# Performance work log

Measured on AMD Instinct MI355X. Metric: run time of the kernel, lower is better.

Reference implementation:

```python
import jax, jax.numpy as jnp
import numpy as np

N_HEAD = 12

def setup_inputs() -> dict:
    key = jax.random.key(0)
    k1, k2, k3 = jax.random.split(key, 3)
    B, T, C = 8, 1024, 768
    x = jax.random.normal(k1, (B, T, C), dtype=jnp.float32)
    # torch nn.Linear weight layout: [out_features, in_features]
    W_attn = jax.random.normal(k2, (3 * C, C), dtype=jnp.float32) * 0.02
    b_attn = jax.random.normal(k3, (3 * C,), dtype=jnp.float32) * 0.02
    return {"x": x, "W_attn": W_attn, "b_attn": b_attn}

def reference(x, W_attn, b_attn):
    B, T, C = x.shape
    H = N_HEAD
    hs = C // H
    scale = 1.0 / jnp.sqrt(jnp.asarray(hs, x.dtype))
    # fused qkv projection: x @ W^T + b  -> [B, T, 3C]
    qkv = jnp.einsum('btc,oc->bto', x, W_attn) + b_attn
    qkv = qkv.reshape(B, T, 3, H, hs).transpose(2, 0, 3, 1, 4)  # [3, B, H, T, hs]
    q, k, v = qkv[0], qkv[1], qkv[2]
    scores = jnp.einsum('bhqd,bhkd->bhqk', q, k) * scale  # [B, H, T, T]
    causal = jnp.tril(jnp.ones((T, T), dtype=bool))
    # masked_fill(-inf) followed by ReLU == zero out masked positions after ReLU
    att = jnp.where(causal, jax.nn.relu(scores), jnp.zeros((), scores.dtype))
    y = jnp.einsum('bhqk,bhkd->bhqd', att, v)  # [B, H, T, hs]
    return y.transpose(0, 2, 1, 3).reshape(B, T, C)
```

## Files before the change

kernel.cpp:

```cpp
#include <hip/hip_runtime.h>
#include <hip/hip_bf16.h>
#include <stdint.h>

#define T_ 1024
#define C_ 768
#define H_ 12
#define HS 64

typedef __attribute__((ext_vector_type(8))) short bf16x8;
typedef __attribute__((ext_vector_type(4))) float f32x4;
typedef __attribute__((ext_vector_type(16))) float f32x16;

#define GLOAD16(g, l) __builtin_amdgcn_global_load_lds( \
    (const __attribute__((address_space(1))) uint32_t*)(g), \
    (__attribute__((address_space(3))) uint32_t*)(l), 16, 0, 0)

#define WAITCNT_VM(n) asm volatile("s_waitcnt vmcnt(" #n ")" ::: "memory")

__device__ __forceinline__ ushort f2b(float f) {
  uint32_t u = __builtin_bit_cast(uint32_t, f);
  u = (u + 0x7fffu + ((u >> 16) & 1u)) >> 16;
  return (ushort)u;
}

__device__ __forceinline__ uint cvtpk(float a, float b) {
  uint r;
  asm("v_cvt_pk_bf16_f32 %0, %1, %2" : "=v"(r) : "v"(a), "v"(b));
  return r;
}

__global__ __launch_bounds__(256) void cvt_bf16(
    const float* __restrict__ x, const float* __restrict__ wt,
    ushort* __restrict__ xb, ushort* __restrict__ wb) {
  const int NX4 = 8192 * 768 / 4;
  const int NW4 = 2304 * 768 / 4;
  int i = blockIdx.x * 256 + threadIdx.x;
  int stride = gridDim.x * 256;
  for (int idx = i; idx < NX4; idx += stride) {
    float4 f = ((const float4*)x)[idx];
    ushort4 o;
    o.x = f2b(f.x); o.y = f2b(f.y); o.z = f2b(f.z); o.w = f2b(f.w);
    ((ushort4*)xb)[idx] = o;
  }
  for (int idx = i; idx < NW4; idx += stride) {
    float4 f = ((const float4*)wt)[idx];
    ushort4 o;
    o.x = f2b(f.x); o.y = f2b(f.y); o.z = f2b(f.z); o.w = f2b(f.w);
    ((ushort4*)wb)[idx] = o;
  }
}

__global__ __launch_bounds__(256) void qkv_gemm(
    const ushort* __restrict__ xb, const ushort* __restrict__ wb,
    const float* __restrict__ bias,
    ushort* __restrict__ qo, ushort* __restrict__ ko, ushort* __restrict__ vT) {
  __shared__ __align__(16) char smem[81920];
  const int tid = threadIdx.x, lane = tid & 63, w = tid >> 6;
  const int g = lane >> 4, l15 = lane & 15;
  const int id = blockIdx.x;
  const int wg = (id & 7) * 144 + (id >> 3);
  const int m0 = (wg / 18) * 128, n0 = (wg % 18) * 128;
  const int wr = w >> 1, wc = w & 1;
  f32x4 acc[4][4] = {};

  const ushort* srcA[2];
  const ushort* srcB[2];
  int dstoff[2];
  #pragma unroll
  for (int c = 0; c < 2; ++c) {
    int p = (c * 4 + w) * 64 + lane;
    int row = p >> 2, s = p & 3;
    int sc = (s ^ ((row >> 1) & 3)) * 8;
    srcA[c] = xb + (size_t)(m0 + row) * 768 + sc;
    srcB[c] = wb + (size_t)(n0 + row) * 768 + sc;
    dstoff[c] = (c * 4 + w) * 1024;
  }

#define STAGE_G(bb_, k0) do { \
    _Pragma("unroll") \
    for (int c_ = 0; c_ < 2; ++c_) { \
      GLOAD16(srcA[c_] + (k0), (bb_) + dstoff[c_]); \
      GLOAD16(srcB[c_] + (k0), (bb_) + 8192 + dstoff[c_]); \
    } \
  } while (0)

#define GEMM_COMPUTE(cb_) do { \
    bf16x8 af[4], bfr[4]; \
    _Pragma("unroll") \
    for (int mi = 0; mi < 4; ++mi) { \
      int r_ = wr * 64 + mi * 16 + l15; \
      af[mi] = *(const bf16x8*)((cb_) + r_ * 64 + ((g ^ ((r_ >> 1) & 3)) << 4)); \
    } \
    _Pragma("unroll") \
    for (int ni = 0; ni < 4; ++ni) { \
      int r_ = wc * 64 + ni * 16 + l15; \
      bfr[ni] = *(const bf16x8*)((cb_) + 8192 + r_ * 64 + ((g ^ ((r_ >> 1) & 3)) << 4)); \
    } \
    __builtin_amdgcn_s_setprio(1); \
    _Pragma("unroll") \
    for (int mi = 0; mi < 4; ++mi) \
      _Pragma("unroll") \
      for (int ni = 0; ni < 4; ++ni) \
        acc[mi][ni] = __builtin_amdgcn_mfma_f32_16x16x32_bf16(af[mi], bfr[ni], acc[mi][ni], 0, 0, 0); \
    __builtin_amdgcn_s_setprio(0); \
  } while (0)

  STAGE_G(smem, 0);
  STAGE_G(smem + 16384, 32);
  STAGE_G(smem + 32768, 64);
  STAGE_G(smem + 49152, 96);
  char* cptr = smem;
  char* sptr = smem + 65536;
  for (int kk = 0; kk < 23; ++kk) {
    if (kk <= 20)      WAITCNT_VM(12);
    else if (kk == 21) WAITCNT_VM(8);
    else               WAITCNT_VM(4);
    __builtin_amdgcn_s_barrier();
    if (kk < 20) STAGE_G(sptr, (kk + 4) * 32);
    GEMM_COMPUTE(cptr);
    cptr += 16384; if (cptr == smem + 81920) cptr = smem;
    sptr += 16384; if (sptr == smem + 81920) sptr = smem;
  }
  WAITCNT_VM(0);
  __builtin_amdgcn_s_barrier();
  GEMM_COMPUTE(cptr);
  __syncthreads();

  const int which = n0 / 768;
  if (which < 2) {
    ushort* outp = (which == 0) ? qo : ko;
    #pragma unroll
    for (int ni = 0; ni < 4; ++ni) {
      float bn = bias[n0 + wc * 64 + ni * 16 + l15];
      int nl = wc * 64 + ni * 16 + l15;
      #pragma unroll
      for (int mi = 0; mi < 4; ++mi) {
        #pragma unroll
        for (int r = 0; r < 4; ++r) {
          int ml = wr * 64 + mi * 16 + g * 4 + r;
          *(ushort*)(smem + ml * 256 + ((nl * 2) ^ ((ml & 7) << 4))) =
              f2b(acc[mi][ni][r] + bn);
        }
      }
    }
    __syncthreads();
    #pragma unroll
    for (int c = 0; c < 8; ++c) {
      int p = c * 256 + tid;
      int ml = p >> 4, nch = p & 15;
      uint4 val = *(const uint4*)(smem + ml * 256 + ((nch * 16) ^ ((ml & 7) << 4)));
      int m = m0 + ml;
      int nin = n0 + nch * 8 - which * 768;
      int h = nin >> 6, d = nin & 63;
      *(uint4*)(outp + ((size_t)((m >> 10) * H_ + h) * T_ + (m & (T_ - 1))) * HS + d) = val;
    }
  } else {
    #pragma unroll
    for (int ni = 0; ni < 4; ++ni) {
      float bn = bias[n0 + wc * 64 + ni * 16 + l15];
      int dl = wc * 64 + ni * 16 + l15;
      #pragma unroll
      for (int mi = 0; mi < 4; ++mi) {
        #pragma unroll
        for (int r = 0; r < 4; ++r) {
          int tl = wr * 64 + mi * 16 + g * 4 + r;
          *(ushort*)(smem + dl * 256 + ((tl * 2) ^ ((dl & 7) << 4))) =
              f2b(acc[mi][ni][r] + bn);
        }
      }
    }
    __syncthreads();
    const int b = m0 >> 10, t0base = m0 & 1023;
    #pragma unroll
    for (int c = 0; c < 8; ++c) {
      int p = c * 256 + tid;
      int dl = p >> 4, tch = p & 15;
      uint4 val = *(const uint4*)(smem + dl * 256 + ((tch * 16) ^ ((dl & 7) << 4)));
      int nin = n0 + dl - 1536;
      int h = nin >> 6, dd = nin & 63;
      *(uint4*)(vT + (((size_t)(b * H_ + h) * HS + dd) << 10) + t0base + tch * 8) = val;
    }
  }
}

__global__ __launch_bounds__(512, 4) void attn_relu(
    const ushort* __restrict__ q, const ushort* __restrict__ k,
    const ushort* __restrict__ vT, float* __restrict__ out) {
  __shared__ __align__(16) char smem[49152];
  const int tid = threadIdx.x, lane = tid & 63, w = tid >> 6;
  const int l31 = lane & 31, h = lane >> 5;
  const int raw = blockIdx.x;
  const int chunk = 3 - (raw / 96);
  const int bh = raw % 96;
  const size_t base = (size_t)bh * (T_ * HS);
  const int q0w = chunk * 256 + w * 32;
  const int nkt = chunk * 4 + 4;

  bf16x8 qf[4];
  #pragma unroll
  for (int s = 0; s < 4; ++s)
    qf[s] = *(const bf16x8*)(q + base + (size_t)(q0w + l31) * HS + s * 16 + h * 8);

  const int rowS = tid >> 3;
  const int colS = ((tid & 7) ^ (rowS & 7)) * 8;
  const int dstS = tid * 16;

#define STAGE_KV(bb_, kt) do { \
    GLOAD16(k  + base + (size_t)((kt) * 64 + rowS) * HS + colS, (bb_) + dstS); \
    GLOAD16(vT + base + (size_t)rowS * T_ + (kt) * 64 + colS, (bb_) + 8192 + dstS); \
  } while (0)

  f32x16 yacc0 = {}, yacc1 = {};

#define ATTN_TILE(cb_, kt) do { \
    const char* Kb = (cb_); \
    const char* Vb = (cb_) + 8192; \
    _Pragma("unroll") \
    for (int kr = 0; kr < 2; ++kr) { \
      int kbase = (kt) * 64 + kr * 32; \
      if (kbase <= q0w + 31) { \
        f32x16 sacc = {}; \
        int arow = kr * 32 + l31; \
        __builtin_amdgcn_s_setprio(1); \
        _Pragma("unroll") \
        for (int s = 0; s < 4; ++s) { \
          bf16x8 kf = *(const bf16x8*)(Kb + arow * 128 + (((2 * s + h) ^ (arow & 7)) << 4)); \
          sacc = __builtin_amdgcn_mfma_f32_32x32x16_bf16(kf, qf[s], sacc, 0, 0, 0); \
        } \
        __builtin_amdgcn_s_setprio(0); \
        const bool fullk = (kbase + 31 <= q0w); \
        uint wds[8]; \
        _Pragma("unroll") \
        for (int i = 0; i < 8; ++i) { \
          float a = fmaxf(sacc[2 * i] * 0.125f, 0.0f); \
          float b = fmaxf(sacc[2 * i + 1] * 0.125f, 0.0f); \
          if (!fullk) { \
            int r0 = 2 * i, r1 = 2 * i + 1; \
            if (kbase + (r0 & 3) + 8 * (r0 >> 2) + 4 * h > q0w + l31) a = 0.0f; \
            if (kbase + (r1 & 3) + 8 * (r1 >> 2) + 4 * h > q0w + l31) b = 0.0f; \
          } \
          wds[i] = cvtpk(a, b); \
        } \
        __builtin_amdgcn_s_setprio(1); \
        _Pragma("unroll") \
        for (int t = 0; t < 2; ++t) { \
          int4 pw = { (int)wds[4 * t], (int)wds[4 * t + 1], \
                      (int)wds[4 * t + 2], (int)wds[4 * t + 3] }; \
          bf16x8 pa = __builtin_bit_cast(bf16x8, pw); \
          _Pragma("unroll") \
          for (int dt = 0; dt < 2; ++dt) { \
            int d = dt * 32 + l31; \
            uint2 lo = *(const uint2*)(Vb + d * 128 + (((4 * kr + 2 * t) ^ (d & 7)) << 4) + 8 * h); \
            uint2 hi = *(const uint2*)(Vb + d * 128 + (((4 * kr + 2 * t + 1) ^ (d & 7)) << 4) + 8 * h); \
            int4 vv = { (int)lo.x, (int)lo.y, (int)hi.x, (int)hi.y }; \
            bf16x8 vf = __builtin_bit_cast(bf16x8, vv); \
            if (dt == 0) yacc0 = __builtin_amdgcn_mfma_f32_32x32x16_bf16(pa, vf, yacc0, 0, 0, 0); \
            else         yacc1 = __builtin_amdgcn_mfma_f32_32x32x16_bf16(pa, vf, yacc1, 0, 0, 0); \
          } \
        } \
        __builtin_amdgcn_s_setprio(0); \
      } \
    } \
  } while (0)

  STAGE_KV(smem, 0);
  if (nkt > 1) STAGE_KV(smem + 16384, 1);
  char* cptr = smem;
  char* sptr = smem + 32768;
  for (int kt = 0; kt < nkt - 1; ++kt) {
    WAITCNT_VM(2);
    __builtin_amdgcn_s_barrier();
    if (kt + 2 < nkt) STAGE_KV(sptr, kt + 2);
    ATTN_TILE(cptr, kt);
    cptr += 16384; if (cptr == smem + 49152) cptr = smem;
    sptr += 16384; if (sptr == smem + 49152) sptr = smem;
  }
  WAITCNT_VM(0);
  __builtin_amdgcn_s_barrier();
  ATTN_TILE(cptr, nkt - 1);

  const int bb = bh / H_, hh = bh % H_;
  #pragma unroll
  for (int r = 0; r < 16; ++r) {
    int qrow = q0w + (r & 3) + 8 * (r >> 2) + 4 * h;
    float* op = out + (size_t)(bb * T_ + qrow) * C_ + hh * HS;
    op[l31] = yacc0[r];
    op[32 + l31] = yacc1[r];
  }
}

extern "C" void kernel_launch(void* const* d_in, const int* in_sizes, int n_in,
                              void* d_out, int out_size, void* d_ws, size_t ws_size,
                              hipStream_t stream) {
  const float* x    = (const float*)d_in[0];
  const float* W    = (const float*)d_in[1];
  const float* bias = (const float*)d_in[2];
  float* out = (float*)d_out;

  char* ws = (char*)d_ws;
  ushort* xb = (ushort*)ws;
  ushort* wb = (ushort*)(ws + 12582912);
  ushort* qb = (ushort*)(ws + 16121856);
  ushort* kb = (ushort*)(ws + 28704768);
  ushort* vT = (ushort*)(ws + 41287680);

  cvt_bf16<<<2048, 256, 0, stream>>>(x, W, xb, wb);
  qkv_gemm<<<1152, 256, 0, stream>>>(xb, wb, bias, qb, kb, vT);
  attn_relu<<<384, 512, 0, stream>>>(qb, kb, vT, out);
}
```

Measured before the change: 153.5 us.

## Widen QKV GEMM tile to 128x256 with 512 threads and 3-stage pipeline

New measurement: 148.5 us. -3.3%, faster.

```diff
diff --git a/kernel.cpp b/kernel.cpp
--- a/kernel.cpp
+++ b/kernel.cpp
@@ -50,38 +50,38 @@
   }
 }
 
-__global__ __launch_bounds__(256) void qkv_gemm(
+__global__ __launch_bounds__(512, 4) void qkv_gemm(
     const ushort* __restrict__ xb, const ushort* __restrict__ wb,
     const float* __restrict__ bias,
     ushort* __restrict__ qo, ushort* __restrict__ ko, ushort* __restrict__ vT) {
-  __shared__ __align__(16) char smem[81920];
+  __shared__ __align__(16) char smem[73728];
   const int tid = threadIdx.x, lane = tid & 63, w = tid >> 6;
   const int g = lane >> 4, l15 = lane & 15;
   const int id = blockIdx.x;
-  const int wg = (id & 7) * 144 + (id >> 3);
-  const int m0 = (wg / 18) * 128, n0 = (wg % 18) * 128;
-  const int wr = w >> 1, wc = w & 1;
+  const int wg = (id & 7) * 72 + (id >> 3);
+  const int m0 = (wg / 9) * 128, n0 = (wg % 9) * 256;
+  const int wr = w >> 2, wc = w & 3;
   f32x4 acc[4][4] = {};
 
-  const ushort* srcA[2];
+  const ushort* srcA;
   const ushort* srcB[2];
-  int dstoff[2];
+  int dstA, dstB[2];
+  {
+    int p = tid, row = p >> 2, s = p & 3;
+    srcA = xb + (size_t)(m0 + row) * 768 + (s ^ ((row >> 1) & 3)) * 8;
+    dstA = p * 16;
+  }
   #pragma unroll
   for (int c = 0; c < 2; ++c) {
-    int p = (c * 4 + w) * 64 + lane;
-    int row = p >> 2, s = p & 3;
-    int sc = (s ^ ((row >> 1) & 3)) * 8;
-    srcA[c] = xb + (size_t)(m0 + row) * 768 + sc;
-    srcB[c] = wb + (size_t)(n0 + row) * 768 + sc;
-    dstoff[c] = (c * 4 + w) * 1024;
+    int p = c * 512 + tid, row = p >> 2, s = p & 3;
+    srcB[c] = wb + (size_t)(n0 + row) * 768 + (s ^ ((row >> 1) & 3)) * 8;
+    dstB[c] = 8192 + p * 16;
   }
 
 #define STAGE_G(bb_, k0) do { \
-    _Pragma("unroll") \
-    for (int c_ = 0; c_ < 2; ++c_) { \
-      GLOAD16(srcA[c_] + (k0), (bb_) + dstoff[c_]); \
-      GLOAD16(srcB[c_] + (k0), (bb_) + 8192 + dstoff[c_]); \
-    } \
+    GLOAD16(srcA + (k0), (bb_) + dstA); \
+    GLOAD16(srcB[0] + (k0), (bb_) + dstB[0]); \
+    GLOAD16(srcB[1] + (k0), (bb_) + dstB[1]); \
   } while (0)
 
 #define GEMM_COMPUTE(cb_) do { \
@@ -106,24 +106,18 @@
   } while (0)
 
   STAGE_G(smem, 0);
-  STAGE_G(smem + 16384, 32);
-  STAGE_G(smem + 32768, 64);
-  STAGE_G(smem + 49152, 96);
+  STAGE_G(smem + 24576, 32);
   char* cptr = smem;
-  char* sptr = smem + 65536;
-  for (int kk = 0; kk < 23; ++kk) {
-    if (kk <= 20)      WAITCNT_VM(12);
-    else if (kk == 21) WAITCNT_VM(8);
-    else               WAITCNT_VM(4);
+  char* sptr = smem + 49152;
+  for (int kk = 0; kk < 24; ++kk) {
+    if (kk < 23) WAITCNT_VM(3);
+    else         WAITCNT_VM(0);
     __builtin_amdgcn_s_barrier();
-    if (kk < 20) STAGE_G(sptr, (kk + 4) * 32);
+    if (kk < 22) STAGE_G(sptr, (kk + 2) * 32);
     GEMM_COMPUTE(cptr);
-    cptr += 16384; if (cptr == smem + 81920) cptr = smem;
-    sptr += 16384; if (sptr == smem + 81920) sptr = smem;
-  }
-  WAITCNT_VM(0);
-  __builtin_amdgcn_s_barrier();
-  GEMM_COMPUTE(cptr);
+    cptr += 24576; if (cptr == smem + 73728) cptr = smem;
+    sptr += 24576; if (sptr == smem + 73728) sptr = smem;
+  }
   __syncthreads();
 
   const int which = n0 / 768;
@@ -131,14 +125,14 @@
     ushort* outp = (which == 0) ? qo : ko;
     #pragma unroll
     for (int ni = 0; ni < 4; ++ni) {
-      float bn = bias[n0 + wc * 64 + ni * 16 + l15];
       int nl = wc * 64 + ni * 16 + l15;
+      float bn = bias[n0 + nl];
       #pragma unroll
       for (int mi = 0; mi < 4; ++mi) {
         #pragma unroll
         for (int r = 0; r < 4; ++r) {
           int ml = wr * 64 + mi * 16 + g * 4 + r;
-          *(ushort*)(smem + ml * 256 + ((nl * 2) ^ ((ml & 7) << 4))) =
+          *(ushort*)(smem + ml * 512 + ((nl * 2) ^ ((ml & 7) << 4))) =
               f2b(acc[mi][ni][r] + bn);
         }
       }
@@ -146,9 +140,9 @@
     __syncthreads();
     #pragma unroll
     for (int c = 0; c < 8; ++c) {
-      int p = c * 256 + tid;
-      int ml = p >> 4, nch = p & 15;
-      uint4 val = *(const uint4*)(smem + ml * 256 + ((nch * 16) ^ ((ml & 7) << 4)));
+      int p = c * 512 + tid;
+      int ml = p >> 5, nch = p & 31;
+      uint4 val = *(const uint4*)(smem + ml * 512 + ((nch * 16) ^ ((ml & 7) << 4)));
       int m = m0 + ml;
       int nin = n0 + nch * 8 - which * 768;
       int h = nin >> 6, d = nin & 63;
@@ -157,8 +151,8 @@
   } else {
     #pragma unroll
     for (int ni = 0; ni < 4; ++ni) {
-      float bn = bias[n0 + wc * 64 + ni * 16 + l15];
       int dl = wc * 64 + ni * 16 + l15;
+      float bn = bias[n0 + dl];
       #pragma unroll
       for (int mi = 0; mi < 4; ++mi) {
         #pragma unroll
@@ -173,7 +167,7 @@
     const int b = m0 >> 10, t0base = m0 & 1023;
     #pragma unroll
     for (int c = 0; c < 8; ++c) {
-      int p = c * 256 + tid;
+      int p = c * 512 + tid;
       int dl = p >> 4, tch = p & 15;
       uint4 val = *(const uint4*)(smem + dl * 256 + ((tch * 16) ^ ((dl & 7) << 4)));
       int nin = n0 + dl - 1536;
@@ -305,6 +299,6 @@
   ushort* vT = (ushort*)(ws + 41287680);
 
   cvt_bf16<<<2048, 256, 0, stream>>>(x, W, xb, wb);
-  qkv_gemm<<<1152, 256, 0, stream>>>(xb, wb, bias, qb, kb, vT);
+  qkv_gemm<<<576, 512, 0, stream>>>(xb, wb, bias, qb, kb, vT);
   attn_relu<<<384, 512, 0, stream>>>(qb, kb, vT, out);
 }
```

## Shrink QKV GEMM LDS pipeline to double-buffered 64-wide K tiles for two blocks per CU

Applied to the files above, without the earlier changes.

New measurement: 150.7 us. About the same (-1.8%).

```diff
diff --git a/kernel.cpp b/kernel.cpp
--- a/kernel.cpp
+++ b/kernel.cpp
@@ -50,11 +50,11 @@
   }
 }
 
-__global__ __launch_bounds__(256) void qkv_gemm(
+__global__ __launch_bounds__(256, 2) void qkv_gemm(
     const ushort* __restrict__ xb, const ushort* __restrict__ wb,
     const float* __restrict__ bias,
     ushort* __restrict__ qo, ushort* __restrict__ ko, ushort* __restrict__ vT) {
-  __shared__ __align__(16) char smem[81920];
+  __shared__ __align__(16) char smem[65536];
   const int tid = threadIdx.x, lane = tid & 63, w = tid >> 6;
   const int g = lane >> 4, l15 = lane & 15;
   const int id = blockIdx.x;
@@ -63,38 +63,39 @@
   const int wr = w >> 1, wc = w & 1;
   f32x4 acc[4][4] = {};
 
-  const ushort* srcA[2];
-  const ushort* srcB[2];
-  int dstoff[2];
+  const ushort* sA[2];
+  const ushort* sB[2];
+  int sdst[2];
   #pragma unroll
   for (int c = 0; c < 2; ++c) {
-    int p = (c * 4 + w) * 64 + lane;
-    int row = p >> 2, s = p & 3;
-    int sc = (s ^ ((row >> 1) & 3)) * 8;
-    srcA[c] = xb + (size_t)(m0 + row) * 768 + sc;
-    srcB[c] = wb + (size_t)(n0 + row) * 768 + sc;
-    dstoff[c] = (c * 4 + w) * 1024;
-  }
-
-#define STAGE_G(bb_, k0) do { \
+    int i = c * 256 + tid, r = i >> 2, s = i & 3;
+    int sc = (s ^ ((r >> 1) & 3)) * 8;
+    sA[c] = xb + (size_t)(m0 + r) * 768 + sc;
+    sB[c] = wb + (size_t)(n0 + r) * 768 + sc;
+    sdst[c] = i * 16;
+  }
+
+#define STAGE(bufp_, kd, t) do { \
     _Pragma("unroll") \
     for (int c_ = 0; c_ < 2; ++c_) { \
-      GLOAD16(srcA[c_] + (k0), (bb_) + dstoff[c_]); \
-      GLOAD16(srcB[c_] + (k0), (bb_) + 8192 + dstoff[c_]); \
+      GLOAD16(sA[c_] + (t) * 64 + (kd) * 32, (bufp_) + (kd) * 8192 + sdst[c_]); \
+      GLOAD16(sB[c_] + (t) * 64 + (kd) * 32, (bufp_) + 16384 + (kd) * 8192 + sdst[c_]); \
     } \
   } while (0)
 
-#define GEMM_COMPUTE(cb_) do { \
+#define COMPUTE(bufp_, kd) do { \
+    const char* Ab = (bufp_) + (kd) * 8192; \
+    const char* Bb = Ab + 16384; \
     bf16x8 af[4], bfr[4]; \
     _Pragma("unroll") \
     for (int mi = 0; mi < 4; ++mi) { \
       int r_ = wr * 64 + mi * 16 + l15; \
-      af[mi] = *(const bf16x8*)((cb_) + r_ * 64 + ((g ^ ((r_ >> 1) & 3)) << 4)); \
+      af[mi] = *(const bf16x8*)(Ab + r_ * 64 + ((g ^ ((r_ >> 1) & 3)) << 4)); \
     } \
     _Pragma("unroll") \
     for (int ni = 0; ni < 4; ++ni) { \
       int r_ = wc * 64 + ni * 16 + l15; \
-      bfr[ni] = *(const bf16x8*)((cb_) + 8192 + r_ * 64 + ((g ^ ((r_ >> 1) & 3)) << 4)); \
+      bfr[ni] = *(const bf16x8*)(Bb + r_ * 64 + ((g ^ ((r_ >> 1) & 3)) << 4)); \
     } \
     __builtin_amdgcn_s_setprio(1); \
     _Pragma("unroll") \
@@ -105,25 +106,21 @@
     __builtin_amdgcn_s_setprio(0); \
   } while (0)
 
-  STAGE_G(smem, 0);
-  STAGE_G(smem + 16384, 32);
-  STAGE_G(smem + 32768, 64);
-  STAGE_G(smem + 49152, 96);
-  char* cptr = smem;
-  char* sptr = smem + 65536;
-  for (int kk = 0; kk < 23; ++kk) {
-    if (kk <= 20)      WAITCNT_VM(12);
-    else if (kk == 21) WAITCNT_VM(8);
-    else               WAITCNT_VM(4);
+  STAGE(smem, 0, 0);
+  STAGE(smem, 1, 0);
+  #pragma unroll 2
+  for (int t = 0; t < 12; ++t) {
+    char* cur = smem + (t & 1) * 32768;
+    char* nxt = smem + ((t + 1) & 1) * 32768;
+    WAITCNT_VM(4);
     __builtin_amdgcn_s_barrier();
-    if (kk < 20) STAGE_G(sptr, (kk + 4) * 32);
-    GEMM_COMPUTE(cptr);
-    cptr += 16384; if (cptr == smem + 81920) cptr = smem;
-    sptr += 16384; if (sptr == smem + 81920) sptr = smem;
-  }
-  WAITCNT_VM(0);
-  __builtin_amdgcn_s_barrier();
-  GEMM_COMPUTE(cptr);
+    if (t < 11) STAGE(nxt, 0, t + 1);
+    COMPUTE(cur, 0);
+    if (t < 11) { WAITCNT_VM(4); } else { WAITCNT_VM(0); }
+    __builtin_amdgcn_s_barrier();
+    if (t < 11) STAGE(nxt, 1, t + 1);
+    COMPUTE(cur, 1);
+  }
   __syncthreads();
 
   const int which = n0 / 768;
```
